# Performance work log

Measured on AMD Instinct MI355X. Metric: run time of the kernel, lower is better.

The kernel has to match this reference:

```python
import jax, jax.numpy as jnp
import numpy as np

N_NODES = 100000
N_EDGES = 1600000
D_IN = 128
D_HID = 128
D_OUT = 1


def setup_inputs() -> dict:
    key = jax.random.key(0)
    ks = jax.random.split(key, 8)
    x = jax.random.normal(ks[0], (N_NODES, D_IN), dtype=jnp.float32)
    edge_index = jax.random.randint(ks[1], (2, N_EDGES), 0, N_NODES, dtype=jnp.int64)
    s1 = 1.0 / np.sqrt(D_IN)
    s2 = 1.0 / np.sqrt(D_HID)
    W1 = jax.random.uniform(ks[2], (D_IN, D_HID), jnp.float32, -s1, s1)
    b1 = jnp.zeros((D_HID,), jnp.float32)
    W2 = jax.random.uniform(ks[3], (D_HID, D_HID), jnp.float32, -s2, s2)
    b2 = jnp.zeros((D_HID,), jnp.float32)
    Wl = jax.random.uniform(ks[4], (D_HID, D_OUT), jnp.float32, -s2, s2)
    bl = jax.random.uniform(ks[5], (D_OUT,), jnp.float32, -s2, s2)
    return {"x": x, "edge_index": edge_index, "W1": W1, "b1": b1,
            "W2": W2, "b2": b2, "Wl": Wl, "bl": bl}


def _gcn_norm(edge_index, num_nodes):
    # Add self-loops, compute symmetric normalization 1/sqrt(deg_s * deg_d).
    loops = jnp.arange(num_nodes, dtype=edge_index.dtype)
    src = jnp.concatenate([edge_index[0], loops])
    dst = jnp.concatenate([edge_index[1], loops])
    deg = jax.ops.segment_sum(jnp.ones_like(dst, dtype=jnp.float32), dst,
                              num_segments=num_nodes)
    dinv = jnp.where(deg > 0, jax.lax.rsqrt(deg), 0.0)
    norm = dinv[src] * dinv[dst]  # [E + N]
    return src, dst, norm


def _gcn_conv(h, W, b, src, dst, norm, num_nodes):
    h = h @ W                                  # [N, d_out]
    msg = h[src] * norm[:, None]               # [E+N, d_out] gather
    out = jax.ops.segment_sum(msg, dst, num_segments=num_nodes)  # scatter-add
    return out + b


def reference(x, edge_index, W1, b1, W2, b2, Wl, bl):
    num_nodes = x.shape[0]
    src, dst, norm = _gcn_norm(edge_index, num_nodes)
    h = jax.nn.relu(_gcn_conv(x, W1, b1, src, dst, norm, num_nodes))
    # dropout is identity in eval mode
    h = jax.nn.relu(_gcn_conv(h, W2, b2, src, dst, norm, num_nodes))
    return h @ Wl + bl
```

## Files before the change

### kernel.cpp

```cpp
#include <hip/hip_runtime.h>

#define DHID 128
#define BCAP 10240
#define PCHUNK 4096
#define XS_LD 136
#define SMEM_PART 21504
#define SMEM_MID  17408

typedef _Float16 h4 __attribute__((ext_vector_type(4)));
typedef _Float16 h8 __attribute__((ext_vector_type(8)));
typedef float    f32x4 __attribute__((ext_vector_type(4)));

__device__ inline void hoist_afrag_f16(const _Float16* __restrict__ Wt, int w, int l16, int lq,
                                       h8 afrag[2][4]) {
#pragma unroll
    for (int ct = 0; ct < 2; ++ct) {
        int c = w * 32 + ct * 16 + l16;
#pragma unroll
        for (int kb = 0; kb < 4; ++kb)
            afrag[ct][kb] = *(const h8*)(Wt + (size_t)c * DHID + kb * 32 + lq * 8);
    }
}

__device__ inline void wtrans_body(const float* __restrict__ W, _Float16* __restrict__ Wt) {
    int t = threadIdx.x;
    int c = t & 127, k0 = (t >> 7) * 64;
#pragma unroll
    for (int kb = 0; kb < 8; ++kb) {
        h8 v;
#pragma unroll
        for (int j = 0; j < 8; ++j)
            v[j] = (_Float16)W[(size_t)(k0 + kb * 8 + j) * DHID + c];
        *(h8*)(Wt + (size_t)c * DHID + k0 + kb * 8) = v;
    }
}

__device__ inline void partition_body(char* smem, const int* __restrict__ ei, int E, int nbuck,
                                      int* __restrict__ bcur, unsigned* __restrict__ packed, int blk) {
    unsigned* sdata = (unsigned*)smem;
    int* lcnt  = (int*)(smem + 16384);
    int* lbase = (int*)(smem + 17408);
    int* loff  = (int*)(smem + 18432);
    int* lcur  = (int*)(smem + 19456);
    int* sscan = (int*)(smem + 20480);
    int t = threadIdx.x;
    int e0 = blk * PCHUNK;
    lcnt[t] = 0;
    __syncthreads();

    int sreg[16], dreg[16];
#pragma unroll
    for (int k = 0; k < 16; ++k) {
        int e = e0 + t + k * 256;
        if (e < E) { sreg[k] = ei[e]; dreg[k] = ei[E + e]; }
        else dreg[k] = -1;
    }

#pragma unroll
    for (int k = 0; k < 16; ++k)
        if (dreg[k] >= 0) atomicAdd(&lcnt[dreg[k] >> 9], 1);
    __syncthreads();

    int c = lcnt[t];
    sscan[t] = c;
    __syncthreads();
    for (int off = 1; off < 256; off <<= 1) {
        int v = (t >= off) ? sscan[t - off] : 0;
        __syncthreads();
        sscan[t] += v;
        __syncthreads();
    }
    loff[t] = sscan[t] - c;
    if (t < nbuck && c > 0) lbase[t] = atomicAdd(&bcur[t], c);
    lcur[t] = sscan[t] - c;
    __syncthreads();

#pragma unroll
    for (int k = 0; k < 16; ++k) {
        if (dreg[k] >= 0) {
            int b = dreg[k] >> 9;
            int pos = atomicAdd(&lcur[b], 1);
            sdata[pos] = ((unsigned)(dreg[k] & 511) << 17) | (unsigned)sreg[k];
        }
    }
    __syncthreads();

    int wid = t >> 6, lane = t & 63;
    for (int b = wid; b < nbuck; b += 4) {
        int cb = lcnt[b];
        if (cb == 0) continue;
        int gbase = b * BCAP + lbase[b];
        int sbase = loff[b];
        for (int k = lane; k < cb; k += 64) packed[gbase + k] = sdata[sbase + k];
    }
}

__global__ __launch_bounds__(256) void k_part(const int* __restrict__ ei, int E, int nbuck,
                                              int* __restrict__ bcur, unsigned* __restrict__ packed,
                                              const float* __restrict__ W1, const float* __restrict__ W2,
                                              _Float16* __restrict__ W1t, _Float16* __restrict__ W2t,
                                              int nPart) {
    __shared__ __align__(16) char smem[SMEM_PART];
    int b = blockIdx.x;
    if (b < nPart)            partition_body(smem, ei, E, nbuck, bcur, packed, b);
    else if (b == nPart)      wtrans_body(W1, W1t);
    else                      wtrans_body(W2, W2t);
}

__device__ inline void p2b_body(char* smem, const unsigned* __restrict__ packed,
                                const int* __restrict__ bcur,
                                int* __restrict__ row_ptr, float* __restrict__ dinv,
                                int* __restrict__ csr, int nbuck, int N, int E, int b) {
    int* c512   = (int*)smem;
    int* cur512 = (int*)(smem + 2048);
    int* sscan  = (int*)(smem + 4096);
    int* sbk    = (int*)(smem + 5120);
    int t = threadIdx.x;
    sbk[t] = (t < nbuck) ? bcur[t] : 0;
    c512[t] = 0; c512[t + 256] = 0;
    __syncthreads();
    for (int off = 1; off < 256; off <<= 1) {
        int v = (t >= off) ? sbk[t - off] : 0;
        __syncthreads();
        sbk[t] += v;
        __syncthreads();
    }
    int rbase = (b > 0) ? sbk[b - 1] : 0;
    int m = bcur[b];
    const unsigned* pb = packed + (size_t)b * BCAP;
    for (int i = t; i < m; i += 256) atomicAdd(&c512[pb[i] >> 17], 1);
    __syncthreads();
    int v0 = c512[2 * t], v1 = c512[2 * t + 1];
    int ps = v0 + v1;
    sscan[t] = ps;
    __syncthreads();
    for (int off = 1; off < 256; off <<= 1) {
        int v = (t >= off) ? sscan[t - off] : 0;
        __syncthreads();
        sscan[t] += v;
        __syncthreads();
    }
    int excl = sscan[t] - ps;
    cur512[2 * t] = excl;
    cur512[2 * t + 1] = excl + v0;

    int n0 = (b << 9) + 2 * t;
    if (n0 < N) {
        row_ptr[n0] = rbase + excl;
        dinv[n0] = rsqrtf((float)(v0 + 1));
    }
    if (n0 + 1 < N) {
        row_ptr[n0 + 1] = rbase + excl + v0;
        dinv[n0 + 1] = rsqrtf((float)(v1 + 1));
    }
    if (b == 0 && t == 0) row_ptr[N] = E;
    __syncthreads();

    for (int i = t; i < m; i += 256) {
        unsigned p = pb[i];
        int dl = p >> 17;
        int src = (int)(p & 0x1FFFFu);
        int pos = atomicAdd(&cur512[dl], 1);
        csr[rbase + pos] = src;
    }
}

__device__ inline void gemm1_body(char* smem, const float* __restrict__ X,
                                  const _Float16* __restrict__ W1t,
                                  _Float16* __restrict__ Th, int N, int blk) {
    _Float16* Xs = (_Float16*)smem;
    int t = threadIdx.x;
    int w = t >> 6, l = t & 63, l16 = l & 15, lq = l >> 4;

    h8 afrag[2][4];
    hoist_afrag_f16(W1t, w, l16, lq, afrag);

    int rs = t >> 2, cs = (t & 3) * 32;
    int r0 = blk * 64;
    {
        int rg = r0 + rs; if (rg > N - 1) rg = N - 1;
        _Float16* sp = Xs + rs * XS_LD + cs;
        const float* xp = X + (size_t)rg * DHID + cs;
#pragma unroll
        for (int k = 0; k < 4; ++k) {
            float4 a = *(const float4*)(xp + k * 8);
            float4 b = *(const float4*)(xp + k * 8 + 4);
            h8 v;
            v[0] = (_Float16)a.x; v[1] = (_Float16)a.y;
            v[2] = (_Float16)a.z; v[3] = (_Float16)a.w;
            v[4] = (_Float16)b.x; v[5] = (_Float16)b.y;
            v[6] = (_Float16)b.z; v[7] = (_Float16)b.w;
            *(h8*)(sp + k * 8) = v;
        }
    }
    __syncthreads();

    f32x4 acc[4][2];
#pragma unroll
    for (int rt = 0; rt < 4; ++rt)
#pragma unroll
        for (int ct = 0; ct < 2; ++ct) acc[rt][ct] = (f32x4){0.f, 0.f, 0.f, 0.f};

#pragma unroll
    for (int rt = 0; rt < 4; ++rt) {
        const _Float16* bp = Xs + (rt * 16 + l16) * XS_LD + lq * 8;
#pragma unroll
        for (int kb = 0; kb < 4; ++kb) {
            h8 b = *(const h8*)(bp + kb * 32);
            acc[rt][0] = __builtin_amdgcn_mfma_f32_16x16x32_f16(afrag[0][kb], b, acc[rt][0], 0, 0, 0);
            acc[rt][1] = __builtin_amdgcn_mfma_f32_16x16x32_f16(afrag[1][kb], b, acc[rt][1], 0, 0, 0);
        }
    }

#pragma unroll
    for (int rt = 0; rt < 4; ++rt) {
        int r = r0 + rt * 16 + l16;
        if (r < N) {
#pragma unroll
            for (int ct = 0; ct < 2; ++ct) {
                h4 v;
#pragma unroll
                for (int j = 0; j < 4; ++j) v[j] = (_Float16)acc[rt][ct][j];
                *(h4*)(Th + (size_t)r * DHID + w * 32 + ct * 16 + lq * 4) = v;
            }
        }
    }
}

__global__ __launch_bounds__(256) void k_mid(const unsigned* __restrict__ packed,
                                             const int* __restrict__ bcur,
                                             int* __restrict__ row_ptr, float* __restrict__ dinv,
                                             int* __restrict__ csr, int nbuck, int N, int E,
                                             const float* __restrict__ X,
                                             const _Float16* __restrict__ W1t,
                                             _Float16* __restrict__ Th) {
    __shared__ __align__(16) char smem[SMEM_MID];
    int b = blockIdx.x;
    if (b < nbuck)
        p2b_body(smem, packed, bcur, row_ptr, dinv, csr, nbuck, N, E, b);
    else
        gemm1_body(smem, X, W1t, Th, N, b - nbuck);
}

__global__ __launch_bounds__(256) void k_agg_mid(const _Float16* __restrict__ Th,
                                                 const int* __restrict__ row_ptr,
                                                 const int* __restrict__ csr,
                                                 const float* __restrict__ dinv,
                                                 const float* __restrict__ bias,
                                                 _Float16* __restrict__ H, int N) {
    int node = blockIdx.x * 16 + (threadIdx.x >> 4);
    int sl = threadIdx.x & 15;
    if (node >= N) return;

    int e = row_ptr[node];
    int end = row_ptr[node + 1];
    const h8* Tl = (const h8*)Th + sl;

    float acc[8];
#pragma unroll
    for (int c = 0; c < 8; ++c) acc[c] = 0.f;

    for (; e + 4 <= end; e += 4) {
        int s0 = csr[e], s1 = csr[e + 1], s2 = csr[e + 2], s3 = csr[e + 3];
        float d0 = dinv[s0], d1 = dinv[s1], d2 = dinv[s2], d3 = dinv[s3];
        h8 v0 = Tl[(size_t)s0 * 16];
        h8 v1 = Tl[(size_t)s1 * 16];
        h8 v2 = Tl[(size_t)s2 * 16];
        h8 v3 = Tl[(size_t)s3 * 16];
#pragma unroll
        for (int c = 0; c < 8; ++c) {
            float a0 = fmaf(d0, (float)v0[c], fmaf(d1, (float)v1[c], 0.f));
            float a1 = fmaf(d2, (float)v2[c], fmaf(d3, (float)v3[c], 0.f));
            acc[c] += a0 + a1;
        }
    }
    for (; e < end; ++e) {
        int s0 = csr[e];
        float d0 = dinv[s0];
        h8 va = Tl[(size_t)s0 * 16];
#pragma unroll
        for (int c = 0; c < 8; ++c) acc[c] = fmaf(d0, (float)va[c], acc[c]);
    }

    float dn = dinv[node];
    {
        h8 tv = Tl[(size_t)node * 16];
#pragma unroll
        for (int c = 0; c < 8; ++c) acc[c] = fmaf(dn, (float)tv[c], acc[c]);
    }

    const float* bp = bias + sl * 8;
    float4 b0 = *(const float4*)bp;
    float4 b1 = *(const float4*)(bp + 4);
    h8 hv;
    hv[0] = (_Float16)fmaxf(fmaf(dn, acc[0], b0.x), 0.f);
    hv[1] = (_Float16)fmaxf(fmaf(dn, acc[1], b0.y), 0.f);
    hv[2] = (_Float16)fmaxf(fmaf(dn, acc[2], b0.z), 0.f);
    hv[3] = (_Float16)fmaxf(fmaf(dn, acc[3], b0.w), 0.f);
    hv[4] = (_Float16)fmaxf(fmaf(dn, acc[4], b1.x), 0.f);
    hv[5] = (_Float16)fmaxf(fmaf(dn, acc[5], b1.y), 0.f);
    hv[6] = (_Float16)fmaxf(fmaf(dn, acc[6], b1.z), 0.f);
    hv[7] = (_Float16)fmaxf(fmaf(dn, acc[7], b1.w), 0.f);
    *(h8*)(H + (size_t)node * DHID + sl * 8) = hv;
}

__global__ __launch_bounds__(256) void k_gemm_l2(const _Float16* __restrict__ H,
                                                 const _Float16* __restrict__ W2t,
                                                 _Float16* __restrict__ Th2, int N) {
    __shared__ _Float16 Xs[64 * XS_LD];
    int t = threadIdx.x;
    int w = t >> 6, l = t & 63, l16 = l & 15, lq = l >> 4;

    h8 afrag[2][4];
    hoist_afrag_f16(W2t, w, l16, lq, afrag);

    int rs = t >> 2, cs = (t & 3) * 32;
    int r0 = blockIdx.x * 64;
    {
        int rg = r0 + rs; if (rg > N - 1) rg = N - 1;
        _Float16* sp = Xs + rs * XS_LD + cs;
        const _Float16* xp = H + (size_t)rg * DHID + cs;
#pragma unroll
        for (int k = 0; k < 4; ++k)
            *(h8*)(sp + k * 8) = *(const h8*)(xp + k * 8);
    }
    __syncthreads();

    f32x4 acc[4][2];
#pragma unroll
    for (int rt = 0; rt < 4; ++rt)
#pragma unroll
        for (int ct = 0; ct < 2; ++ct) acc[rt][ct] = (f32x4){0.f, 0.f, 0.f, 0.f};

#pragma unroll
    for (int rt = 0; rt < 4; ++rt) {
        const _Float16* bp = Xs + (rt * 16 + l16) * XS_LD + lq * 8;
#pragma unroll
        for (int kb = 0; kb < 4; ++kb) {
            h8 b = *(const h8*)(bp + kb * 32);
            acc[rt][0] = __builtin_amdgcn_mfma_f32_16x16x32_f16(afrag[0][kb], b, acc[rt][0], 0, 0, 0);
            acc[rt][1] = __builtin_amdgcn_mfma_f32_16x16x32_f16(afrag[1][kb], b, acc[rt][1], 0, 0, 0);
        }
    }

#pragma unroll
    for (int rt = 0; rt < 4; ++rt) {
        int r = r0 + rt * 16 + l16;
        if (r < N) {
#pragma unroll
            for (int ct = 0; ct < 2; ++ct) {
                h4 v;
#pragma unroll
                for (int j = 0; j < 4; ++j) v[j] = (_Float16)acc[rt][ct][j];
                *(h4*)(Th2 + (size_t)r * DHID + w * 32 + ct * 16 + lq * 4) = v;
            }
        }
    }
}

__global__ __launch_bounds__(256) void k_agg_fin(const _Float16* __restrict__ Th2,
                                                 const int* __restrict__ row_ptr,
                                                 const int* __restrict__ csr,
                                                 const float* __restrict__ dinv,
                                                 const float* __restrict__ bias,
                                                 const float* __restrict__ Wl,
                                                 const float* __restrict__ bl,
                                                 float* __restrict__ out, int N) {
    int node = blockIdx.x * 16 + (threadIdx.x >> 4);
    int sl = threadIdx.x & 15;
    if (node >= N) return;

    int e = row_ptr[node];
    int end = row_ptr[node + 1];
    const h8* Tl = (const h8*)Th2 + sl;

    float acc[8];
#pragma unroll
    for (int c = 0; c < 8; ++c) acc[c] = 0.f;

    for (; e + 4 <= end; e += 4) {
        int s0 = csr[e], s1 = csr[e + 1], s2 = csr[e + 2], s3 = csr[e + 3];
        float d0 = dinv[s0], d1 = dinv[s1], d2 = dinv[s2], d3 = dinv[s3];
        h8 v0 = Tl[(size_t)s0 * 16];
        h8 v1 = Tl[(size_t)s1 * 16];
        h8 v2 = Tl[(size_t)s2 * 16];
        h8 v3 = Tl[(size_t)s3 * 16];
#pragma unroll
        for (int c = 0; c < 8; ++c) {
            float a0 = fmaf(d0, (float)v0[c], fmaf(d1, (float)v1[c], 0.f));
            float a1 = fmaf(d2, (float)v2[c], fmaf(d3, (float)v3[c], 0.f));
            acc[c] += a0 + a1;
        }
    }
    for (; e < end; ++e) {
        int s0 = csr[e];
        float d0 = dinv[s0];
        h8 va = Tl[(size_t)s0 * 16];
#pragma unroll
        for (int c = 0; c < 8; ++c) acc[c] = fmaf(d0, (float)va[c], acc[c]);
    }

    float dn = dinv[node];
    {
        h8 tv = Tl[(size_t)node * 16];
#pragma unroll
        for (int c = 0; c < 8; ++c) acc[c] = fmaf(dn, (float)tv[c], acc[c]);
    }

    const float* bp = bias + sl * 8;
    float4 b0 = *(const float4*)bp;
    float4 b1 = *(const float4*)(bp + 4);
    float r[8];
    r[0] = fmaxf(fmaf(dn, acc[0], b0.x), 0.f);
    r[1] = fmaxf(fmaf(dn, acc[1], b0.y), 0.f);
    r[2] = fmaxf(fmaf(dn, acc[2], b0.z), 0.f);
    r[3] = fmaxf(fmaf(dn, acc[3], b0.w), 0.f);
    r[4] = fmaxf(fmaf(dn, acc[4], b1.x), 0.f);
    r[5] = fmaxf(fmaf(dn, acc[5], b1.y), 0.f);
    r[6] = fmaxf(fmaf(dn, acc[6], b1.z), 0.f);
    r[7] = fmaxf(fmaf(dn, acc[7], b1.w), 0.f);

    const float* wp = Wl + sl * 8;
    float4 w0 = *(const float4*)wp;
    float4 w1 = *(const float4*)(wp + 4);
    float p = r[0] * w0.x + r[1] * w0.y + r[2] * w0.z + r[3] * w0.w +
              r[4] * w1.x + r[5] * w1.y + r[6] * w1.z + r[7] * w1.w;
#pragma unroll
    for (int off = 8; off > 0; off >>= 1) p += __shfl_down(p, off, 16);
    if (sl == 0) out[node] = p + bl[0];
}

extern "C" void kernel_launch(void* const* d_in, const int* in_sizes, int n_in,
                              void* d_out, int out_size, void* d_ws, size_t ws_size,
                              hipStream_t stream) {
    const float* x  = (const float*)d_in[0];
    const int*   ei = (const int*)d_in[1];
    const float* W1 = (const float*)d_in[2];
    const float* b1 = (const float*)d_in[3];
    const float* W2 = (const float*)d_in[4];
    const float* b2 = (const float*)d_in[5];
    const float* Wl = (const float*)d_in[6];
    const float* bl = (const float*)d_in[7];
    float* out = (float*)d_out;

    int N = in_sizes[0] / DHID;
    int E = in_sizes[1] / 2;
    int nbuck = (N + 511) / 512;
    int nRB = (N + 63) / 64;
    int nPart = (E + PCHUNK - 1) / PCHUNK;

    char* ws = (char*)d_ws;
    size_t off = 0;
    auto alloc = [&](size_t bytes) -> void* {
        void* p = ws + off;
        off += (bytes + 255) & ~(size_t)255;
        return p;
    };
    float*    dinv     = (float*)alloc((size_t)N * 4);
    int*      row_ptr  = (int*)alloc((size_t)(N + 1) * 4);
    int*      bcur     = (int*)alloc((size_t)nbuck * 4);
    int*      csr      = (int*)alloc((size_t)E * 4);
    unsigned* packed   = (unsigned*)alloc((size_t)nbuck * BCAP * 4);
    _Float16* Th       = (_Float16*)alloc((size_t)N * DHID * 2);
    _Float16* Th2      = (_Float16*)alloc((size_t)N * DHID * 2);
    _Float16* H        = (_Float16*)alloc((size_t)N * DHID * 2);
    _Float16* W1t      = (_Float16*)alloc((size_t)DHID * DHID * 2);
    _Float16* W2t      = (_Float16*)alloc((size_t)DHID * DHID * 2);

    (void)hipMemsetAsync(bcur, 0, (size_t)nbuck * 4, stream);

    k_part<<<nPart + 2, 256, 0, stream>>>(ei, E, nbuck, bcur, packed, W1, W2, W1t, W2t, nPart);
    k_mid<<<nbuck + nRB, 256, 0, stream>>>(packed, bcur, row_ptr, dinv, csr, nbuck, N, E,
                                           x, W1t, Th);
    k_agg_mid<<<(N + 15) / 16, 256, 0, stream>>>(Th, row_ptr, csr, dinv, b1, H, N);
    k_gemm_l2<<<nRB, 256, 0, stream>>>(H, W2t, Th2, N);
    k_agg_fin<<<(N + 15) / 16, 256, 0, stream>>>(Th2, row_ptr, csr, dinv, b2, Wl, bl, out, N);
}
```

Baseline: 200.8 us.

## Fuse layer-2 GEMM into final aggregation by aggregating before transform

Removes the separate layer-2 GEMM kernel and the Th2 buffer. It uses linearity to aggregate H first and then multiply by W2 inside the final aggregation kernel. The product uses MFMA with W2 staged in shared memory per block, and ds_bpermute rearranges the aggregated rows into B fragments. This drops one kernel launch and a full N×128 fp16 write and read. In exchange, every block loads 32KB of W2 into LDS, which may limit occupancy, and the gather-aggregate now reads H instead of Th2.

```diff
diff --git a/kernel.cpp b/kernel.cpp
--- a/kernel.cpp
+++ b/kernel.cpp
@@ -4,12 +4,14 @@
 #define BCAP 10240
 #define PCHUNK 4096
 #define XS_LD 136
+#define W2_LD 132
 #define SMEM_PART 21504
 #define SMEM_MID  17408
 
 typedef _Float16 h4 __attribute__((ext_vector_type(4)));
 typedef _Float16 h8 __attribute__((ext_vector_type(8)));
 typedef float    f32x4 __attribute__((ext_vector_type(4)));
+typedef int      i32x4 __attribute__((ext_vector_type(4)));
 
 __device__ inline void hoist_afrag_f16(const _Float16* __restrict__ Wt, int w, int l16, int lq,
                                        h8 afrag[2][4]) {
@@ -304,75 +306,35 @@
     *(h8*)(H + (size_t)node * DHID + sl * 8) = hv;
 }
 
-__global__ __launch_bounds__(256) void k_gemm_l2(const _Float16* __restrict__ H,
-                                                 const _Float16* __restrict__ W2t,
-                                                 _Float16* __restrict__ Th2, int N) {
-    __shared__ _Float16 Xs[64 * XS_LD];
-    int t = threadIdx.x;
-    int w = t >> 6, l = t & 63, l16 = l & 15, lq = l >> 4;
-
-    h8 afrag[2][4];
-    hoist_afrag_f16(W2t, w, l16, lq, afrag);
-
-    int rs = t >> 2, cs = (t & 3) * 32;
-    int r0 = blockIdx.x * 64;
-    {
-        int rg = r0 + rs; if (rg > N - 1) rg = N - 1;
-        _Float16* sp = Xs + rs * XS_LD + cs;
-        const _Float16* xp = H + (size_t)rg * DHID + cs;
-#pragma unroll
-        for (int k = 0; k < 4; ++k)
-            *(h8*)(sp + k * 8) = *(const h8*)(xp + k * 8);
-    }
-    __syncthreads();
-
-    f32x4 acc[4][2];
-#pragma unroll
-    for (int rt = 0; rt < 4; ++rt)
-#pragma unroll
-        for (int ct = 0; ct < 2; ++ct) acc[rt][ct] = (f32x4){0.f, 0.f, 0.f, 0.f};
-
-#pragma unroll
-    for (int rt = 0; rt < 4; ++rt) {
-        const _Float16* bp = Xs + (rt * 16 + l16) * XS_LD + lq * 8;
-#pragma unroll
-        for (int kb = 0; kb < 4; ++kb) {
-            h8 b = *(const h8*)(bp + kb * 32);
-            acc[rt][0] = __builtin_amdgcn_mfma_f32_16x16x32_f16(afrag[0][kb], b, acc[rt][0], 0, 0, 0);
-            acc[rt][1] = __builtin_amdgcn_mfma_f32_16x16x32_f16(afrag[1][kb], b, acc[rt][1], 0, 0, 0);
-        }
-    }
-
-#pragma unroll
-    for (int rt = 0; rt < 4; ++rt) {
-        int r = r0 + rt * 16 + l16;
-        if (r < N) {
-#pragma unroll
-            for (int ct = 0; ct < 2; ++ct) {
-                h4 v;
-#pragma unroll
-                for (int j = 0; j < 4; ++j) v[j] = (_Float16)acc[rt][ct][j];
-                *(h4*)(Th2 + (size_t)r * DHID + w * 32 + ct * 16 + lq * 4) = v;
-            }
-        }
-    }
-}
-
-__global__ __launch_bounds__(256) void k_agg_fin(const _Float16* __restrict__ Th2,
+__global__ __launch_bounds__(256) void k_agg_fin(const _Float16* __restrict__ H,
                                                  const int* __restrict__ row_ptr,
                                                  const int* __restrict__ csr,
                                                  const float* __restrict__ dinv,
-                                                 const float* __restrict__ bias,
+                                                 const float* __restrict__ b2,
+                                                 const _Float16* __restrict__ W2t,
                                                  const float* __restrict__ Wl,
                                                  const float* __restrict__ bl,
                                                  float* __restrict__ out, int N) {
-    int node = blockIdx.x * 16 + (threadIdx.x >> 4);
-    int sl = threadIdx.x & 15;
-    if (node >= N) return;
-
-    int e = row_ptr[node];
-    int end = row_ptr[node + 1];
-    const h8* Tl = (const h8*)Th2 + sl;
+    __shared__ _Float16 W2s[DHID * W2_LD];
+    int t = threadIdx.x;
+    {
+        int r = t >> 1, hh = (t & 1) * 64;
+        const _Float16* src = W2t + (size_t)r * DHID + hh;
+        _Float16* dst = W2s + r * W2_LD + hh;
+#pragma unroll
+        for (int k = 0; k < 8; ++k)
+            *(h8*)(dst + k * 8) = *(const h8*)(src + k * 8);
+    }
+    __syncthreads();
+
+    int node = blockIdx.x * 16 + (t >> 4);
+    int sl = t & 15;
+    bool gvalid = node < N;
+    int nc = gvalid ? node : N - 1;
+    int e = row_ptr[nc];
+    int end = row_ptr[nc + 1];
+    if (!gvalid) end = e;
+    const h8* Tl = (const h8*)H + sl;
 
     float acc[8];
 #pragma unroll
@@ -400,34 +362,57 @@
         for (int c = 0; c < 8; ++c) acc[c] = fmaf(d0, (float)va[c], acc[c]);
     }
 
-    float dn = dinv[node];
+    float dn = gvalid ? dinv[nc] : 0.f;
     {
-        h8 tv = Tl[(size_t)node * 16];
+        h8 tv = Tl[(size_t)nc * 16];
 #pragma unroll
         for (int c = 0; c < 8; ++c) acc[c] = fmaf(dn, (float)tv[c], acc[c]);
     }
 
-    const float* bp = bias + sl * 8;
-    float4 b0 = *(const float4*)bp;
-    float4 b1 = *(const float4*)(bp + 4);
-    float r[8];
-    r[0] = fmaxf(fmaf(dn, acc[0], b0.x), 0.f);
-    r[1] = fmaxf(fmaf(dn, acc[1], b0.y), 0.f);
-    r[2] = fmaxf(fmaf(dn, acc[2], b0.z), 0.f);
-    r[3] = fmaxf(fmaf(dn, acc[3], b0.w), 0.f);
-    r[4] = fmaxf(fmaf(dn, acc[4], b1.x), 0.f);
-    r[5] = fmaxf(fmaf(dn, acc[5], b1.y), 0.f);
-    r[6] = fmaxf(fmaf(dn, acc[6], b1.z), 0.f);
-    r[7] = fmaxf(fmaf(dn, acc[7], b1.w), 0.f);
-
-    const float* wp = Wl + sl * 8;
-    float4 w0 = *(const float4*)wp;
-    float4 w1 = *(const float4*)(wp + 4);
-    float p = r[0] * w0.x + r[1] * w0.y + r[2] * w0.z + r[3] * w0.w +
-              r[4] * w1.x + r[5] * w1.y + r[6] * w1.z + r[7] * w1.w;
-#pragma unroll
-    for (int off = 8; off > 0; off >>= 1) p += __shfl_down(p, off, 16);
-    if (sl == 0) out[node] = p + bl[0];
+    h8 gv;
+#pragma unroll
+    for (int c = 0; c < 8; ++c) gv[c] = (_Float16)(dn * acc[c]);
+
+    int l = t & 63;
+    int n = l & 15;
+    int lq = l >> 4;
+    i32x4 gi = *(i32x4*)&gv;
+    h8 bfrag[4];
+    int lbase = (n * 16 + lq) * 4;
+#pragma unroll
+    for (int kb = 0; kb < 4; ++kb) {
+        int idx = lbase + kb * 16;
+        i32x4 bi;
+        bi[0] = __builtin_amdgcn_ds_bpermute(idx, gi[0]);
+        bi[1] = __builtin_amdgcn_ds_bpermute(idx, gi[1]);
+        bi[2] = __builtin_amdgcn_ds_bpermute(idx, gi[2]);
+        bi[3] = __builtin_amdgcn_ds_bpermute(idx, gi[3]);
+        bfrag[kb] = *(h8*)&bi;
+    }
+
+    float p = 0.f;
+#pragma unroll
+    for (int ct = 0; ct < 8; ++ct) {
+        f32x4 d4 = {0.f, 0.f, 0.f, 0.f};
+        const _Float16* ap = W2s + (ct * 16 + n) * W2_LD + lq * 8;
+#pragma unroll
+        for (int kb = 0; kb < 4; ++kb) {
+            h8 a = *(const h8*)(ap + kb * 32);
+            d4 = __builtin_amdgcn_mfma_f32_16x16x32_f16(a, bfrag[kb], d4, 0, 0, 0);
+        }
+        float4 bb = *(const float4*)(b2 + ct * 16 + lq * 4);
+        float4 wl = *(const float4*)(Wl + ct * 16 + lq * 4);
+        p += fmaxf(d4[0] + bb.x, 0.f) * wl.x + fmaxf(d4[1] + bb.y, 0.f) * wl.y +
+             fmaxf(d4[2] + bb.z, 0.f) * wl.z + fmaxf(d4[3] + bb.w, 0.f) * wl.w;
+    }
+    p += __shfl_xor(p, 16, 64);
+    p += __shfl_xor(p, 32, 64);
+
+    if (lq == 0 && n < 4) {
+        int w = t >> 6;
+        int gnode = blockIdx.x * 16 + w * 4 + n;
+        if (gnode < N) out[gnode] = p + bl[0];
+    }
 }
 
 extern "C" void kernel_launch(void* const* d_in, const int* in_sizes, int n_in,
@@ -462,7 +447,6 @@
     int*      csr      = (int*)alloc((size_t)E * 4);
     unsigned* packed   = (unsigned*)alloc((size_t)nbuck * BCAP * 4);
     _Float16* Th       = (_Float16*)alloc((size_t)N * DHID * 2);
-    _Float16* Th2      = (_Float16*)alloc((size_t)N * DHID * 2);
     _Float16* H        = (_Float16*)alloc((size_t)N * DHID * 2);
     _Float16* W1t      = (_Float16*)alloc((size_t)DHID * DHID * 2);
     _Float16* W2t      = (_Float16*)alloc((size_t)DHID * DHID * 2);
@@ -473,6 +457,5 @@
     k_mid<<<nbuck + nRB, 256, 0, stream>>>(packed, bcur, row_ptr, dinv, csr, nbuck, N, E,
                                            x, W1t, Th);
     k_agg_mid<<<(N + 15) / 16, 256, 0, stream>>>(Th, row_ptr, csr, dinv, b1, H, N);
-    k_gemm_l2<<<nRB, 256, 0, stream>>>(H, W2t, Th2, N);
-    k_agg_fin<<<(N + 15) / 16, 256, 0, stream>>>(Th2, row_ptr, csr, dinv, b2, Wl, bl, out, N);
-}
+    k_agg_fin<<<(N + 15) / 16, 256, 0, stream>>>(H, row_ptr, csr, dinv, b2, W2t, Wl, bl, out, N);
+}
```

Result: slower. 275.2 us (+37.0%).
